# Kernel optimization log

Hardware: AMD Instinct MI355X
Metric: run time of the kernel (lower is better)

The kernel has to match this reference:

```python
import jax, jax.numpy as jnp
import numpy as np

N_MODEL = 1024
N_HEADS = 16
KV_HEADS = 4
HEAD_DIM = N_MODEL // N_HEADS          # 64
KV_MODEL = HEAD_DIM * KV_HEADS         # 256
GROUPS = N_HEADS // KV_HEADS           # 4
B, S = 4, 2048


def _rmsnorm(x):
    return x * jax.lax.rsqrt(jnp.mean(x * x, axis=-1, keepdims=True) + 1e-6)


def _act_quant(x):
    # 8-bit absmax per-token quantization (BitNet b1.58)
    scale = 127.0 / jnp.clip(jnp.max(jnp.abs(x), axis=-1, keepdims=True), 1e-5)
    return jnp.clip(jnp.round(x * scale), -128.0, 127.0) / scale


def _weight_quant(w):
    # ternary absmean quantization
    scale = 1.0 / jnp.clip(jnp.mean(jnp.abs(w)), 1e-5)
    return jnp.clip(jnp.round(w * scale), -1.0, 1.0) / scale


def bitlinear(x, w, b):
    xn = _rmsnorm(x)
    xq = xn + jax.lax.stop_gradient(_act_quant(xn) - xn)   # STE
    wq = w + jax.lax.stop_gradient(_weight_quant(w) - w)   # STE
    return jnp.einsum('...i,oi->...o', xq, wq) + b


def setup_inputs() -> dict:
    key = jax.random.key(0)
    ks = jax.random.split(key, 11)
    sq = 1.0 / np.sqrt(N_MODEL)
    sk = 1.0 / np.sqrt(KV_MODEL)
    return {
        'query': jax.random.normal(ks[0], (B, S, N_MODEL), jnp.float32),
        'key':   jax.random.normal(ks[1], (B, S, N_MODEL), jnp.float32),
        'value': jax.random.normal(ks[2], (B, S, N_MODEL), jnp.float32),
        'Wq': jax.random.normal(ks[3], (N_MODEL, N_MODEL), jnp.float32) * sq,
        'bq': jnp.zeros((N_MODEL,), jnp.float32),
        'Wk': jax.random.normal(ks[4], (KV_MODEL, N_MODEL), jnp.float32) * sq,
        'bk': jnp.zeros((KV_MODEL,), jnp.float32),
        'Wv': jax.random.normal(ks[5], (KV_MODEL, N_MODEL), jnp.float32) * sq,
        'bv': jnp.zeros((KV_MODEL,), jnp.float32),
        'Wo': jax.random.normal(ks[6], (N_MODEL, KV_MODEL), jnp.float32) * sk,
        'bo': jnp.zeros((N_MODEL,), jnp.float32),
    }


def reference(query, key, value, Wq, bq, Wk, bk, Wv, bv, Wo, bo):
    b = query.shape[0]
    Q = bitlinear(query, Wq, bq)   # [b, n, n_model]
    K = bitlinear(key,   Wk, bk)   # [b, s, kv_model]
    V = bitlinear(value, Wv, bv)   # [b, s, kv_model]

    # [b, h, n, d] layouts
    Q = Q.reshape(b, -1, N_HEADS, HEAD_DIM).transpose(0, 2, 1, 3)
    K = K.reshape(b, -1, KV_HEADS, HEAD_DIM).transpose(0, 2, 1, 3)
    V = V.reshape(b, -1, KV_HEADS, HEAD_DIM).transpose(0, 2, 1, 3)

    # group query heads: [b, g, kv_h, n, d]
    Qg = Q.reshape(b, KV_HEADS, GROUPS, -1, HEAD_DIM).transpose(0, 2, 1, 3, 4)
    # NOTE: faithful to the module, the einsum output has no 'g' axis,
    # so the grouped query heads are SUMMED over g.
    energy = jnp.einsum('bghnd,bhsd->bhns', Qg, K)  # [b, kv_h, n, s]

    scale = jnp.sqrt(jnp.float32(HEAD_DIM))
    attention = jax.nn.softmax(energy / scale, axis=-1)
    x = jnp.einsum('bhns,bhsd->bhnd', attention, V)  # [b, kv_h, n, d]
    x = x.transpose(0, 2, 1, 3).reshape(b, -1, KV_MODEL)
    x = bitlinear(x, Wo, bo)       # [b, n, n_model]
    return (x, attention)
```

## Files before the change

### kernel.cpp

```cpp
#include <hip/hip_runtime.h>
#include <stdint.h>

#define N_MODELC 1024
#define KV_MODELC 256
#define BATCH 4
#define SEQ 2048
#define NTOK (BATCH*SEQ)
#define NCHUNK 4
#define CHUNK (SEQ/NCHUNK)

typedef __attribute__((ext_vector_type(4))) float f32x4;
typedef __attribute__((ext_vector_type(4))) int   i32x4;
typedef __attribute__((ext_vector_type(8))) short s16x8;
typedef __attribute__((ext_vector_type(4))) short s16x4;

__device__ __forceinline__ unsigned short f2bf(float f){
  unsigned u = __builtin_bit_cast(unsigned, f);
  u = (u + 0x7FFFu + ((u>>16)&1u)) >> 16;
  return (unsigned short)u;
}
__device__ __forceinline__ float bf2f(unsigned short b){
  return __builtin_bit_cast(float, ((unsigned)b)<<16);
}

__global__ __launch_bounds__(256) void k_actquant1024(
    const float* __restrict__ xq_in, const float* __restrict__ xk_in, const float* __restrict__ xv_in,
    int8_t* __restrict__ q8q, int8_t* __restrict__ q8k, int8_t* __restrict__ q8v,
    float* __restrict__ scq, float* __restrict__ sck, float* __restrict__ scv)
{
  int row = blockIdx.x, which = blockIdx.y, t = threadIdx.x;
  const float* x = (which==0)?xq_in:(which==1)?xk_in:xv_in;
  int8_t* q8 = (which==0)?q8q:(which==1)?q8k:q8v;
  float* sc = (which==0)?scq:(which==1)?sck:scv;
  const float* xr = x + (size_t)row*N_MODELC;
  float4 v = reinterpret_cast<const float4*>(xr)[t];
  float ss = v.x*v.x + v.y*v.y + v.z*v.z + v.w*v.w;
  float am = fmaxf(fmaxf(fabsf(v.x),fabsf(v.y)), fmaxf(fabsf(v.z),fabsf(v.w)));
  #pragma unroll
  for (int m=32;m;m>>=1){ ss += __shfl_xor(ss,m,64); am = fmaxf(am, __shfl_xor(am,m,64)); }
  __shared__ float red[8];
  int wid = t>>6;
  if ((t&63)==0){ red[wid]=ss; red[4+wid]=am; }
  __syncthreads();
  ss = red[0]+red[1]+red[2]+red[3];
  am = fmaxf(fmaxf(red[4],red[5]), fmaxf(red[6],red[7]));
  float rinv = rsqrtf(ss*(1.0f/N_MODELC) + 1e-6f);
  float clipv = fmaxf(am*rinv, 1e-5f);
  float qs = 127.0f/clipv;
  float fsc = rinv*qs;
  char4 o;
  o.x = (signed char)(int)fminf(127.f, fmaxf(-128.f, rintf(v.x*fsc)));
  o.y = (signed char)(int)fminf(127.f, fmaxf(-128.f, rintf(v.y*fsc)));
  o.z = (signed char)(int)fminf(127.f, fmaxf(-128.f, rintf(v.z*fsc)));
  o.w = (signed char)(int)fminf(127.f, fmaxf(-128.f, rintf(v.w*fsc)));
  reinterpret_cast<char4*>(q8 + (size_t)row*N_MODELC)[t] = o;
  if (t==0) sc[row] = clipv*(1.0f/127.0f);
}

__global__ __launch_bounds__(64) void k_actquant256(
    const float* __restrict__ X, int8_t* __restrict__ q8, float* __restrict__ sc)
{
  int row = blockIdx.x, l = threadIdx.x;
  float4 v = reinterpret_cast<const float4*>(X + (size_t)row*KV_MODELC)[l];
  float ss = v.x*v.x + v.y*v.y + v.z*v.z + v.w*v.w;
  float am = fmaxf(fmaxf(fabsf(v.x),fabsf(v.y)), fmaxf(fabsf(v.z),fabsf(v.w)));
  #pragma unroll
  for (int m=32;m;m>>=1){ ss += __shfl_xor(ss,m,64); am = fmaxf(am, __shfl_xor(am,m,64)); }
  float rinv = rsqrtf(ss*(1.0f/KV_MODELC) + 1e-6f);
  float clipv = fmaxf(am*rinv, 1e-5f);
  float qs = 127.0f/clipv;
  float fsc = rinv*qs;
  char4 o;
  o.x = (signed char)(int)fminf(127.f, fmaxf(-128.f, rintf(v.x*fsc)));
  o.y = (signed char)(int)fminf(127.f, fmaxf(-128.f, rintf(v.y*fsc)));
  o.z = (signed char)(int)fminf(127.f, fmaxf(-128.f, rintf(v.z*fsc)));
  o.w = (signed char)(int)fminf(127.f, fmaxf(-128.f, rintf(v.w*fsc)));
  reinterpret_cast<char4*>(q8 + (size_t)row*KV_MODELC)[l] = o;
  if (l==0) sc[row] = clipv*(1.0f/127.0f);
}

__global__ __launch_bounds__(256) void k_wabs_partial(
    const float* __restrict__ Wq, const float* __restrict__ Wk,
    const float* __restrict__ Wv, const float* __restrict__ Wo, float* __restrict__ partial)
{
  int mat = blockIdx.y;
  const float* w = (mat==0)?Wq:(mat==1)?Wk:(mat==2)?Wv:Wo;
  int n = (mat==0)?(N_MODELC*N_MODELC):(KV_MODELC*N_MODELC);
  float s = 0.f;
  for (int i = blockIdx.x*256 + threadIdx.x; i < n; i += 256*256) s += fabsf(w[i]);
  #pragma unroll
  for (int m=32;m;m>>=1) s += __shfl_xor(s,m,64);
  __shared__ float red[4];
  int wid = threadIdx.x>>6;
  if ((threadIdx.x&63)==0) red[wid]=s;
  __syncthreads();
  if (threadIdx.x==0) partial[mat*256 + blockIdx.x] = red[0]+red[1]+red[2]+red[3];
}

__global__ __launch_bounds__(256) void k_wfinal(const float* __restrict__ partial, float* __restrict__ wfac)
{
  int mat = blockIdx.x, t = threadIdx.x;
  float s = partial[mat*256 + t];
  #pragma unroll
  for (int m=32;m;m>>=1) s += __shfl_xor(s,m,64);
  __shared__ float red[4];
  int wid = t>>6;
  if ((t&63)==0) red[wid]=s;
  __syncthreads();
  if (t==0){
    float tot = red[0]+red[1]+red[2]+red[3];
    float n = (mat==0)?(float)(N_MODELC*N_MODELC):(float)(KV_MODELC*N_MODELC);
    wfac[mat] = fmaxf(tot/n, 1e-5f);
  }
}

__global__ __launch_bounds__(256) void k_tern(
    const float* __restrict__ Wq, const float* __restrict__ Wk,
    const float* __restrict__ Wv, const float* __restrict__ Wo,
    const float* __restrict__ wfac,
    int8_t* __restrict__ Wqs, int8_t* __restrict__ Wkt,
    int8_t* __restrict__ Wvt, int8_t* __restrict__ Wot)
{
  int mat = blockIdx.y;
  int idx = blockIdx.x*256 + threadIdx.x;
  if (mat==0){
    float s = 1.0f/wfac[0];
    int op = idx>>10, i = idx&1023;
    int kv = op>>6, d = op&63;
    int acc = 0;
    #pragma unroll
    for (int g=0; g<4; g++){
      float w = Wq[(size_t)(kv*256 + g*64 + d)*N_MODELC + i];
      float r = fminf(1.f, fmaxf(-1.f, rintf(w*s)));
      acc += (int)r;
    }
    Wqs[idx] = (int8_t)acc;
  } else {
    const float* w = (mat==1)?Wk:(mat==2)?Wv:Wo;
    int8_t* o = (mat==1)?Wkt:(mat==2)?Wvt:Wot;
    float s = 1.0f/wfac[mat];
    float r = fminf(1.f, fmaxf(-1.f, rintf(w[idx]*s)));
    o[idx] = (int8_t)r;
  }
}

template<int MODE>
__global__ __launch_bounds__(512) void k_gemm_i8_1024(
    const int8_t* __restrict__ A, const int8_t* __restrict__ B,
    const float* __restrict__ rowscale, const float* __restrict__ wfac, int wfi,
    const float* __restrict__ bias, unsigned short* __restrict__ outp)
{
  __shared__ i32x4 redk[4][4][64];
  __shared__ unsigned short tlds[(MODE==2)?64:1][72];
  const int KDIM = 1024;
  int mb = blockIdx.x*64, nb = blockIdx.y*64;
  int w = threadIdx.x>>6, l = threadIdx.x&63, lr = l&15, lk = l>>4;
  int rw = w&3, kh = w>>2;
  const int8_t* Ap = A + (size_t)(mb + rw*16 + lr)*KDIM + kh*512 + lk*16;
  const int8_t* Bp = B + (size_t)(nb + lr)*KDIM + kh*512 + lk*16;
  i32x4 acc[4];
  #pragma unroll
  for (int f=0; f<4; f++) acc[f] = i32x4{0,0,0,0};
  #pragma unroll 4
  for (int kk=0; kk<512; kk+=64){
    i32x4 a = *reinterpret_cast<const i32x4*>(Ap + kk);
    #pragma unroll
    for (int f=0; f<4; f++){
      i32x4 b = *reinterpret_cast<const i32x4*>(Bp + (size_t)f*16*KDIM + kk);
      acc[f] = __builtin_amdgcn_mfma_i32_16x16x64_i8(a, b, acc[f], 0, 0, 0);
    }
  }
  if (kh==1){
    #pragma unroll
    for (int f=0; f<4; f++) redk[rw][f][l] = acc[f];
  }
  __syncthreads();
  if (kh==0){
    float wf = wfac[wfi];
    #pragma unroll
    for (int f=0; f<4; f++){
      acc[f] += redk[rw][f][l];
      int col = nb + f*16 + lr;
      float bval;
      if constexpr (MODE==0){
        int kv = col>>6, d = col&63;
        const float* bb = bias + kv*256 + d;
        bval = bb[0]+bb[64]+bb[128]+bb[192];
      } else {
        bval = bias[col];
      }
      #pragma unroll
      for (int r=0; r<4; r++){
        int row = mb + rw*16 + lk*4 + r;
        float val = (float)acc[f][r] * (rowscale[row]*wf) + bval;
        if constexpr (MODE==0){
          outp[(size_t)row*KV_MODELC + col] = f2bf(0.125f*val);
        } else if constexpr (MODE==1){
          outp[(size_t)row*KV_MODELC + col] = f2bf(val);
        } else {
          tlds[f*16+lr][rw*16 + lk*4 + r] = f2bf(val);
        }
      }
    }
  }
  if constexpr (MODE==2){
    __syncthreads();
    int u = threadIdx.x;
    int col = u>>3, part = u&7;
    int b = mb>>11, s0 = mb&2047;
    s16x8 vv = *reinterpret_cast<const s16x8*>(&tlds[col][part*8]);
    *reinterpret_cast<s16x8*>(&outp[((size_t)(b*256 + nb + col))*SEQ + s0 + part*8]) = vv;
  }
}

__global__ __launch_bounds__(256) void k_gemm_o(
    const int8_t* __restrict__ A, const int8_t* __restrict__ B,
    const float* __restrict__ rowscale, const float* __restrict__ wfac,
    const float* __restrict__ bias, float* __restrict__ outp)
{
  const int KDIM = 256;
  int mb = blockIdx.x*64, nb = blockIdx.y*64;
  int w = threadIdx.x>>6, l = threadIdx.x&63, lr = l&15, lk = l>>4;
  const int8_t* Ap = A + (size_t)(mb + w*16 + lr)*KDIM + lk*16;
  const int8_t* Bp = B + (size_t)(nb + lr)*KDIM + lk*16;
  i32x4 acc[4];
  #pragma unroll
  for (int f=0; f<4; f++) acc[f] = i32x4{0,0,0,0};
  #pragma unroll
  for (int kk=0; kk<KDIM; kk+=64){
    i32x4 a = *reinterpret_cast<const i32x4*>(Ap + kk);
    #pragma unroll
    for (int f=0; f<4; f++){
      i32x4 b = *reinterpret_cast<const i32x4*>(Bp + (size_t)f*16*KDIM + kk);
      acc[f] = __builtin_amdgcn_mfma_i32_16x16x64_i8(a, b, acc[f], 0, 0, 0);
    }
  }
  float wf = wfac[3];
  #pragma unroll
  for (int f=0; f<4; f++){
    int col = nb + f*16 + lr;
    float bval = bias[col];
    #pragma unroll
    for (int r=0; r<4; r++){
      int row = mb + w*16 + lk*4 + r;
      outp[(size_t)row*N_MODELC + col] = (float)acc[f][r]*(rowscale[row]*wf) + bval;
    }
  }
}

__global__ __launch_bounds__(256) void k_attn1(
    const unsigned short* __restrict__ Qs, const unsigned short* __restrict__ Kb,
    float* __restrict__ mpart, float* __restrict__ lpart)
{
  int bkv = blockIdx.y, b = bkv>>2, kv = bkv&3;
  int c = blockIdx.z;
  int w = threadIdx.x>>6, l = threadIdx.x&63, lr = l&15, lk = l>>4;
  int rowt = blockIdx.x*64 + w*16;
  size_t tq = (size_t)(b*SEQ + rowt + lr)*KV_MODELC + kv*64 + lk*8;
  s16x8 qa0 = *reinterpret_cast<const s16x8*>(Qs + tq);
  s16x8 qa1 = *reinterpret_cast<const s16x8*>(Qs + tq + 32);
  const unsigned short* kbase = Kb + (size_t)b*SEQ*KV_MODELC + kv*64 + lk*8;
  float m[4], ll[4];
  #pragma unroll
  for (int r=0;r<4;r++){ m[r] = -INFINITY; ll[r] = 0.f; }
  for (int st=c*CHUNK; st<(c+1)*CHUNK; st+=16){
    const unsigned short* kp = kbase + (size_t)(st+lr)*KV_MODELC;
    s16x8 k0 = *reinterpret_cast<const s16x8*>(kp);
    s16x8 k1 = *reinterpret_cast<const s16x8*>(kp + 32);
    f32x4 acc = {0.f,0.f,0.f,0.f};
    acc = __builtin_amdgcn_mfma_f32_16x16x32_bf16(qa0, k0, acc, 0,0,0);
    acc = __builtin_amdgcn_mfma_f32_16x16x32_bf16(qa1, k1, acc, 0,0,0);
    #pragma unroll
    for (int r=0;r<4;r++){
      float e = acc[r];
      float mn = fmaxf(m[r], e);
      ll[r] = ll[r]*__expf(m[r]-mn) + __expf(e-mn);
      m[r] = mn;
    }
  }
  #pragma unroll
  for (int r=0;r<4;r++){
    #pragma unroll
    for (int mask=1; mask<16; mask<<=1){
      float om = __shfl_xor(m[r], mask, 64);
      float ol = __shfl_xor(ll[r], mask, 64);
      float mn = fmaxf(m[r], om);
      ll[r] = ll[r]*__expf(m[r]-mn) + ol*__expf(om-mn);
      m[r] = mn;
    }
  }
  if (lr==0){
    #pragma unroll
    for (int r=0;r<4;r++){
      size_t idx = ((size_t)(c*16 + bkv))*SEQ + rowt + lk*4 + r;
      mpart[idx] = m[r];
      lpart[idx] = ll[r];
    }
  }
}

__global__ __launch_bounds__(256) void k_attn2(
    const unsigned short* __restrict__ Qs, const unsigned short* __restrict__ Kb,
    const unsigned short* __restrict__ VT,
    const float* __restrict__ mpart, const float* __restrict__ lpart,
    float* __restrict__ attn, float* __restrict__ pvpart)
{
  __shared__ unsigned short plds[64][64];
  int bkv = blockIdx.y, b = bkv>>2, kv = bkv&3;
  int c = blockIdx.z;
  int w = threadIdx.x>>6, l = threadIdx.x&63, lr = l&15, lk = l>>4;
  int brow = blockIdx.x*64;
  int rowt = brow + w*16;
  size_t tq = (size_t)(b*SEQ + rowt + lr)*KV_MODELC + kv*64 + lk*8;
  s16x8 qa0 = *reinterpret_cast<const s16x8*>(Qs + tq);
  s16x8 qa1 = *reinterpret_cast<const s16x8*>(Qs + tq + 32);
  const unsigned short* kbase = Kb + (size_t)b*SEQ*KV_MODELC + kv*64 + lk*8;
  const unsigned short* vbase = VT + ((size_t)(b*256 + kv*64))*SEQ;

  float m[4], invl[4];
  #pragma unroll
  for (int r=0;r<4;r++){
    int row = rowt + lk*4 + r;
    float M = -INFINITY, L = 0.f;
    #pragma unroll
    for (int cc=0; cc<NCHUNK; cc++){
      size_t idx = ((size_t)(cc*16 + bkv))*SEQ + row;
      float mm = mpart[idx], lw = lpart[idx];
      float mn = fmaxf(M, mm);
      L = L*__expf(M-mn) + lw*__expf(mm-mn);
      M = mn;
    }
    m[r] = M; invl[r] = 1.0f/L;
  }

  float* arow = attn + (size_t)bkv*SEQ*SEQ + (size_t)brow*SEQ;
  f32x4 acco[4];
  #pragma unroll
  for (int dt=0; dt<4; dt++) acco[dt] = f32x4{0.f,0.f,0.f,0.f};
  int qw = w*16 + lk*4;
  int qr = w*16 + lr;
  int rsw = (qr&7)<<3;

  for (int st=c*CHUNK; st<(c+1)*CHUNK; st+=64){
    #pragma unroll
    for (int sub=0; sub<4; sub++){
      int s0 = st + sub*16;
      const unsigned short* kp = kbase + (size_t)(s0+lr)*KV_MODELC;
      s16x8 k0 = *reinterpret_cast<const s16x8*>(kp);
      s16x8 k1 = *reinterpret_cast<const s16x8*>(kp + 32);
      f32x4 acc = {0.f,0.f,0.f,0.f};
      acc = __builtin_amdgcn_mfma_f32_16x16x32_bf16(qa0, k0, acc, 0,0,0);
      acc = __builtin_amdgcn_mfma_f32_16x16x32_bf16(qa1, k1, acc, 0,0,0);
      int slocal = sub*16 + lr;
      #pragma unroll
      for (int r=0;r<4;r++){
        float p = __expf(acc[r]-m[r])*invl[r];
        int sw = (slocal & 7) | ((((slocal>>3) ^ ((qw+r)&7)))<<3);
        plds[qw + r][sw] = f2bf(p);
      }
    }
    s16x8 a0 = *reinterpret_cast<const s16x8*>(&plds[qr][(lk<<3) ^ rsw]);
    s16x8 a1 = *reinterpret_cast<const s16x8*>(&plds[qr][((4+lk)<<3) ^ rsw]);
    #pragma unroll
    for (int dt=0; dt<4; dt++){
      const unsigned short* vp = vbase + (size_t)(dt*16+lr)*SEQ + st + lk*8;
      s16x8 b0 = *reinterpret_cast<const s16x8*>(vp);
      s16x8 b1 = *reinterpret_cast<const s16x8*>(vp + 32);
      acco[dt] = __builtin_amdgcn_mfma_f32_16x16x32_bf16(a0, b0, acco[dt], 0,0,0);
      acco[dt] = __builtin_amdgcn_mfma_f32_16x16x32_bf16(a1, b1, acco[dt], 0,0,0);
    }
    #pragma unroll
    for (int j=0; j<4; j++){
      int row = w*16 + j*4 + (l>>4);
      int sseg = l & 15;
      int chunk = sseg >> 1, half = sseg & 1;
      int off = ((chunk ^ (row&7)) << 3) + (half<<2);
      s16x4 pb = *reinterpret_cast<const s16x4*>(&plds[row][off]);
      float4 pv4;
      pv4.x = bf2f((unsigned short)pb[0]);
      pv4.y = bf2f((unsigned short)pb[1]);
      pv4.z = bf2f((unsigned short)pb[2]);
      pv4.w = bf2f((unsigned short)pb[3]);
      *reinterpret_cast<float4*>(&arow[(size_t)row*SEQ + st + sseg*4]) = pv4;
    }
  }
  {
    int T = (bkv*32 + blockIdx.x)*4 + w;
    float* base = pvpart + ((size_t)c*2048 + T)*1024;
    #pragma unroll
    for (int dt=0; dt<4; dt++){
      *reinterpret_cast<f32x4*>(base + (dt*64 + l)*4) = acco[dt];
    }
  }
}

__global__ __launch_bounds__(256) void k_pvsum(
    const float* __restrict__ pvpart, float* __restrict__ X)
{
  __shared__ float xls[16][65];
  int T = blockIdx.x;
  int w = T&3, qblk = (T>>2)&31, bkv = T>>7;
  int b = bkv>>2, kv = bkv&3;
  int t = threadIdx.x;
  int dt = t>>6, l = t&63;
  f32x4 s = {0.f,0.f,0.f,0.f};
  #pragma unroll
  for (int c=0; c<NCHUNK; c++){
    f32x4 v = *reinterpret_cast<const f32x4*>(pvpart + ((size_t)c*2048 + T)*1024 + t*4);
    s += v;
  }
  int lk = l>>4, lr = l&15;
  #pragma unroll
  for (int r=0; r<4; r++) xls[lk*4+r][dt*16+lr] = s[r];
  __syncthreads();
  int row = t>>4, col4 = (t&15)*4;
  float4 o;
  o.x = xls[row][col4]; o.y = xls[row][col4+1];
  o.z = xls[row][col4+2]; o.w = xls[row][col4+3];
  *reinterpret_cast<float4*>(&X[((size_t)(b*SEQ + qblk*64 + w*16 + row))*KV_MODELC + kv*64 + col4]) = o;
}

extern "C" void kernel_launch(void* const* d_in, const int* in_sizes, int n_in,
                              void* d_out, int out_size, void* d_ws, size_t ws_size,
                              hipStream_t stream)
{
  (void)in_sizes; (void)n_in; (void)out_size; (void)ws_size;
  const float* q  = (const float*)d_in[0];
  const float* k  = (const float*)d_in[1];
  const float* v  = (const float*)d_in[2];
  const float* Wq = (const float*)d_in[3];
  const float* bq = (const float*)d_in[4];
  const float* Wk = (const float*)d_in[5];
  const float* bk = (const float*)d_in[6];
  const float* Wv = (const float*)d_in[7];
  const float* bv = (const float*)d_in[8];
  const float* Wo = (const float*)d_in[9];
  const float* bo = (const float*)d_in[10];

  float* out_x = (float*)d_out;
  float* out_attn = out_x + (size_t)NTOK*N_MODELC;

  char* ws = (char*)d_ws;
  size_t off = 0;
  auto alloc = [&](size_t bytes)->void*{
    void* p = ws + off; off += (bytes + 255) & ~(size_t)255; return p;
  };
  int8_t* q8q = (int8_t*)alloc((size_t)NTOK*N_MODELC);
  int8_t* q8k = (int8_t*)alloc((size_t)NTOK*N_MODELC);
  int8_t* q8v = (int8_t*)alloc((size_t)NTOK*N_MODELC);
  int8_t* q8x = (int8_t*)alloc((size_t)NTOK*KV_MODELC);
  float* scq = (float*)alloc(NTOK*4);
  float* sck = (float*)alloc(NTOK*4);
  float* scv = (float*)alloc(NTOK*4);
  float* scx = (float*)alloc(NTOK*4);
  float* partial = (float*)alloc(4*256*4);
  float* wfac = (float*)alloc(256);
  int8_t* Wqs = (int8_t*)alloc(256*1024);
  int8_t* Wkt = (int8_t*)alloc(256*1024);
  int8_t* Wvt = (int8_t*)alloc(256*1024);
  int8_t* Wot = (int8_t*)alloc(1024*256);
  unsigned short* Qs = (unsigned short*)alloc((size_t)NTOK*KV_MODELC*2);
  unsigned short* Kb = (unsigned short*)alloc((size_t)NTOK*KV_MODELC*2);
  unsigned short* VT = (unsigned short*)alloc((size_t)NTOK*KV_MODELC*2);
  float* X = (float*)alloc((size_t)NTOK*KV_MODELC*4);
  float* mpart = (float*)alloc((size_t)NCHUNK*16*SEQ*4);
  float* lpart = (float*)alloc((size_t)NCHUNK*16*SEQ*4);
  float* pvpart = (float*)alloc((size_t)NCHUNK*2048*1024*4);

  hipLaunchKernelGGL(k_actquant1024, dim3(NTOK,3), dim3(256), 0, stream,
                     q,k,v, q8q,q8k,q8v, scq,sck,scv);
  hipLaunchKernelGGL(k_wabs_partial, dim3(256,4), dim3(256), 0, stream, Wq,Wk,Wv,Wo, partial);
  hipLaunchKernelGGL(k_wfinal, dim3(4), dim3(256), 0, stream, partial, wfac);
  hipLaunchKernelGGL(k_tern, dim3(1024,4), dim3(256), 0, stream,
                     Wq,Wk,Wv,Wo, wfac, Wqs,Wkt,Wvt,Wot);
  hipLaunchKernelGGL((k_gemm_i8_1024<0>), dim3(128,4), dim3(512), 0, stream,
                     q8q, Wqs, scq, wfac, 0, bq, Qs);
  hipLaunchKernelGGL((k_gemm_i8_1024<1>), dim3(128,4), dim3(512), 0, stream,
                     q8k, Wkt, sck, wfac, 1, bk, Kb);
  hipLaunchKernelGGL((k_gemm_i8_1024<2>), dim3(128,4), dim3(512), 0, stream,
                     q8v, Wvt, scv, wfac, 2, bv, VT);
  hipLaunchKernelGGL(k_attn1, dim3(32,16,NCHUNK), dim3(256), 0, stream,
                     Qs, Kb, mpart, lpart);
  hipLaunchKernelGGL(k_attn2, dim3(32,16,NCHUNK), dim3(256), 0, stream,
                     Qs, Kb, VT, mpart, lpart, out_attn, pvpart);
  hipLaunchKernelGGL(k_pvsum, dim3(2048), dim3(256), 0, stream, pvpart, X);
  hipLaunchKernelGGL(k_actquant256, dim3(NTOK), dim3(64), 0, stream, X, q8x, scx);
  hipLaunchKernelGGL(k_gemm_o, dim3(128,16), dim3(256), 0, stream,
                     q8x, Wot, scx, wfac, bo, out_x);
}
```

Baseline: 336.3 us.

## Fuse two-pass attention into single pass with fixed softmax shift

```diff
diff --git a/kernel.cpp b/kernel.cpp
--- a/kernel.cpp
+++ b/kernel.cpp
@@ -6,13 +6,13 @@
 #define BATCH 4
 #define SEQ 2048
 #define NTOK (BATCH*SEQ)
-#define NCHUNK 4
-#define CHUNK (SEQ/NCHUNK)
 
 typedef __attribute__((ext_vector_type(4))) float f32x4;
 typedef __attribute__((ext_vector_type(4))) int   i32x4;
 typedef __attribute__((ext_vector_type(8))) short s16x8;
-typedef __attribute__((ext_vector_type(4))) short s16x4;
+
+#define LOG2E 1.4426950408889634f
+#define PSHIFT 32.0f
 
 __device__ __forceinline__ unsigned short f2bf(float f){
   unsigned u = __builtin_bit_cast(unsigned, f);
@@ -248,66 +248,14 @@
   }
 }
 
-__global__ __launch_bounds__(256) void k_attn1(
+__global__ __launch_bounds__(256) void k_attn_fused(
     const unsigned short* __restrict__ Qs, const unsigned short* __restrict__ Kb,
-    float* __restrict__ mpart, float* __restrict__ lpart)
-{
+    const unsigned short* __restrict__ VT, unsigned short* __restrict__ Pws,
+    float* __restrict__ attn, float* __restrict__ X)
+{
+  __shared__ unsigned short plds[64][64];
+  __shared__ float linvl[64];
   int bkv = blockIdx.y, b = bkv>>2, kv = bkv&3;
-  int c = blockIdx.z;
-  int w = threadIdx.x>>6, l = threadIdx.x&63, lr = l&15, lk = l>>4;
-  int rowt = blockIdx.x*64 + w*16;
-  size_t tq = (size_t)(b*SEQ + rowt + lr)*KV_MODELC + kv*64 + lk*8;
-  s16x8 qa0 = *reinterpret_cast<const s16x8*>(Qs + tq);
-  s16x8 qa1 = *reinterpret_cast<const s16x8*>(Qs + tq + 32);
-  const unsigned short* kbase = Kb + (size_t)b*SEQ*KV_MODELC + kv*64 + lk*8;
-  float m[4], ll[4];
-  #pragma unroll
-  for (int r=0;r<4;r++){ m[r] = -INFINITY; ll[r] = 0.f; }
-  for (int st=c*CHUNK; st<(c+1)*CHUNK; st+=16){
-    const unsigned short* kp = kbase + (size_t)(st+lr)*KV_MODELC;
-    s16x8 k0 = *reinterpret_cast<const s16x8*>(kp);
-    s16x8 k1 = *reinterpret_cast<const s16x8*>(kp + 32);
-    f32x4 acc = {0.f,0.f,0.f,0.f};
-    acc = __builtin_amdgcn_mfma_f32_16x16x32_bf16(qa0, k0, acc, 0,0,0);
-    acc = __builtin_amdgcn_mfma_f32_16x16x32_bf16(qa1, k1, acc, 0,0,0);
-    #pragma unroll
-    for (int r=0;r<4;r++){
-      float e = acc[r];
-      float mn = fmaxf(m[r], e);
-      ll[r] = ll[r]*__expf(m[r]-mn) + __expf(e-mn);
-      m[r] = mn;
-    }
-  }
-  #pragma unroll
-  for (int r=0;r<4;r++){
-    #pragma unroll
-    for (int mask=1; mask<16; mask<<=1){
-      float om = __shfl_xor(m[r], mask, 64);
-      float ol = __shfl_xor(ll[r], mask, 64);
-      float mn = fmaxf(m[r], om);
-      ll[r] = ll[r]*__expf(m[r]-mn) + ol*__expf(om-mn);
-      m[r] = mn;
-    }
-  }
-  if (lr==0){
-    #pragma unroll
-    for (int r=0;r<4;r++){
-      size_t idx = ((size_t)(c*16 + bkv))*SEQ + rowt + lk*4 + r;
-      mpart[idx] = m[r];
-      lpart[idx] = ll[r];
-    }
-  }
-}
-
-__global__ __launch_bounds__(256) void k_attn2(
-    const unsigned short* __restrict__ Qs, const unsigned short* __restrict__ Kb,
-    const unsigned short* __restrict__ VT,
-    const float* __restrict__ mpart, const float* __restrict__ lpart,
-    float* __restrict__ attn, float* __restrict__ pvpart)
-{
-  __shared__ unsigned short plds[64][64];
-  int bkv = blockIdx.y, b = bkv>>2, kv = bkv&3;
-  int c = blockIdx.z;
   int w = threadIdx.x>>6, l = threadIdx.x&63, lr = l&15, lk = l>>4;
   int brow = blockIdx.x*64;
   int rowt = brow + w*16;
@@ -316,32 +264,24 @@
   s16x8 qa1 = *reinterpret_cast<const s16x8*>(Qs + tq + 32);
   const unsigned short* kbase = Kb + (size_t)b*SEQ*KV_MODELC + kv*64 + lk*8;
   const unsigned short* vbase = VT + ((size_t)(b*256 + kv*64))*SEQ;
-
-  float m[4], invl[4];
-  #pragma unroll
-  for (int r=0;r<4;r++){
-    int row = rowt + lk*4 + r;
-    float M = -INFINITY, L = 0.f;
-    #pragma unroll
-    for (int cc=0; cc<NCHUNK; cc++){
-      size_t idx = ((size_t)(cc*16 + bkv))*SEQ + row;
-      float mm = mpart[idx], lw = lpart[idx];
-      float mn = fmaxf(M, mm);
-      L = L*__expf(M-mn) + lw*__expf(mm-mn);
-      M = mn;
-    }
-    m[r] = M; invl[r] = 1.0f/L;
-  }
-
-  float* arow = attn + (size_t)bkv*SEQ*SEQ + (size_t)brow*SEQ;
+  unsigned short* pblk = Pws + ((size_t)(bkv*32 + blockIdx.x))*64*SEQ;
+
+  s16x8 ones;
+  #pragma unroll
+  for (int i=0;i<8;i++) ones[i] = (short)0x3F80;
+
   f32x4 acco[4];
   #pragma unroll
   for (int dt=0; dt<4; dt++) acco[dt] = f32x4{0.f,0.f,0.f,0.f};
+  f32x4 accl = {0.f,0.f,0.f,0.f};
+
   int qw = w*16 + lk*4;
   int qr = w*16 + lr;
-  int rsw = (qr&7)<<3;
-
-  for (int st=c*CHUNK; st<(c+1)*CHUNK; st+=64){
+  int rsw = (lr&7)<<3;
+  int rbrow = w*16 + (l>>2);
+  int rbb = l&3;
+
+  for (int st=0; st<SEQ; st+=64){
     #pragma unroll
     for (int sub=0; sub<4; sub++){
       int s0 = st + sub*16;
@@ -354,13 +294,15 @@
       int slocal = sub*16 + lr;
       #pragma unroll
       for (int r=0;r<4;r++){
-        float p = __expf(acc[r]-m[r])*invl[r];
+        float p = exp2f(fmaf(acc[r], LOG2E, -PSHIFT));
         int sw = (slocal & 7) | ((((slocal>>3) ^ ((qw+r)&7)))<<3);
         plds[qw + r][sw] = f2bf(p);
       }
     }
     s16x8 a0 = *reinterpret_cast<const s16x8*>(&plds[qr][(lk<<3) ^ rsw]);
     s16x8 a1 = *reinterpret_cast<const s16x8*>(&plds[qr][((4+lk)<<3) ^ rsw]);
+    accl = __builtin_amdgcn_mfma_f32_16x16x32_bf16(a0, ones, accl, 0,0,0);
+    accl = __builtin_amdgcn_mfma_f32_16x16x32_bf16(a1, ones, accl, 0,0,0);
     #pragma unroll
     for (int dt=0; dt<4; dt++){
       const unsigned short* vp = vbase + (size_t)(dt*16+lr)*SEQ + st + lk*8;
@@ -369,55 +311,52 @@
       acco[dt] = __builtin_amdgcn_mfma_f32_16x16x32_bf16(a0, b0, acco[dt], 0,0,0);
       acco[dt] = __builtin_amdgcn_mfma_f32_16x16x32_bf16(a1, b1, acco[dt], 0,0,0);
     }
-    #pragma unroll
-    for (int j=0; j<4; j++){
-      int row = w*16 + j*4 + (l>>4);
-      int sseg = l & 15;
-      int chunk = sseg >> 1, half = sseg & 1;
-      int off = ((chunk ^ (row&7)) << 3) + (half<<2);
-      s16x4 pb = *reinterpret_cast<const s16x4*>(&plds[row][off]);
-      float4 pv4;
-      pv4.x = bf2f((unsigned short)pb[0]);
-      pv4.y = bf2f((unsigned short)pb[1]);
-      pv4.z = bf2f((unsigned short)pb[2]);
-      pv4.w = bf2f((unsigned short)pb[3]);
-      *reinterpret_cast<float4*>(&arow[(size_t)row*SEQ + st + sseg*4]) = pv4;
-    }
-  }
-  {
-    int T = (bkv*32 + blockIdx.x)*4 + w;
-    float* base = pvpart + ((size_t)c*2048 + T)*1024;
-    #pragma unroll
-    for (int dt=0; dt<4; dt++){
-      *reinterpret_cast<f32x4*>(base + (dt*64 + l)*4) = acco[dt];
-    }
-  }
-}
-
-__global__ __launch_bounds__(256) void k_pvsum(
-    const float* __restrict__ pvpart, float* __restrict__ X)
-{
-  __shared__ float xls[16][65];
-  int T = blockIdx.x;
-  int w = T&3, qblk = (T>>2)&31, bkv = T>>7;
-  int b = bkv>>2, kv = bkv&3;
+    unsigned short* ptile = pblk + (size_t)(st>>6)*4096;
+    #pragma unroll
+    for (int j8=0; j8<2; j8++){
+      int chunk = rbb*2 + j8;
+      s16x8 v = *reinterpret_cast<const s16x8*>(&plds[rbrow][(chunk ^ (rbrow&7))<<3]);
+      *reinterpret_cast<s16x8*>(&ptile[rbrow*64 + chunk*8]) = v;
+    }
+  }
+
+  float invr[4];
+  #pragma unroll
+  for (int r=0;r<4;r++) invr[r] = 1.0f/accl[r];
+  if (lr==0){
+    #pragma unroll
+    for (int r=0;r<4;r++) linvl[w*16 + lk*4 + r] = invr[r];
+  }
+  int token = b*SEQ + rowt + lk*4;
+  #pragma unroll
+  for (int dt=0; dt<4; dt++){
+    #pragma unroll
+    for (int r=0; r<4; r++){
+      X[(size_t)(token + r)*KV_MODELC + kv*64 + dt*16 + lr] = acco[dt][r]*invr[r];
+    }
+  }
+  __syncthreads();
+
+  float* arow = attn + (size_t)bkv*SEQ*SEQ + (size_t)brow*SEQ;
   int t = threadIdx.x;
-  int dt = t>>6, l = t&63;
-  f32x4 s = {0.f,0.f,0.f,0.f};
-  #pragma unroll
-  for (int c=0; c<NCHUNK; c++){
-    f32x4 v = *reinterpret_cast<const f32x4*>(pvpart + ((size_t)c*2048 + T)*1024 + t*4);
-    s += v;
-  }
-  int lk = l>>4, lr = l&15;
-  #pragma unroll
-  for (int r=0; r<4; r++) xls[lk*4+r][dt*16+lr] = s[r];
-  __syncthreads();
-  int row = t>>4, col4 = (t&15)*4;
-  float4 o;
-  o.x = xls[row][col4]; o.y = xls[row][col4+1];
-  o.z = xls[row][col4+2]; o.w = xls[row][col4+3];
-  *reinterpret_cast<float4*>(&X[((size_t)(b*SEQ + qblk*64 + w*16 + row))*KV_MODELC + kv*64 + col4]) = o;
+  const unsigned short* prd = pblk + (size_t)(t>>3)*4096 + (t&7)*8;
+  #pragma unroll 4
+  for (int it=0; it<64; it++){
+    float inv = linvl[it];
+    s16x8 pv = *reinterpret_cast<const s16x8*>(prd + it*64);
+    float4 o0, o1;
+    o0.x = bf2f((unsigned short)pv[0])*inv;
+    o0.y = bf2f((unsigned short)pv[1])*inv;
+    o0.z = bf2f((unsigned short)pv[2])*inv;
+    o0.w = bf2f((unsigned short)pv[3])*inv;
+    o1.x = bf2f((unsigned short)pv[4])*inv;
+    o1.y = bf2f((unsigned short)pv[5])*inv;
+    o1.z = bf2f((unsigned short)pv[6])*inv;
+    o1.w = bf2f((unsigned short)pv[7])*inv;
+    float* dst = &arow[(size_t)it*SEQ + t*8];
+    *reinterpret_cast<float4*>(dst) = o0;
+    *reinterpret_cast<float4*>(dst+4) = o1;
+  }
 }
 
 extern "C" void kernel_launch(void* const* d_in, const int* in_sizes, int n_in,
@@ -463,9 +402,7 @@
   unsigned short* Kb = (unsigned short*)alloc((size_t)NTOK*KV_MODELC*2);
   unsigned short* VT = (unsigned short*)alloc((size_t)NTOK*KV_MODELC*2);
   float* X = (float*)alloc((size_t)NTOK*KV_MODELC*4);
-  float* mpart = (float*)alloc((size_t)NCHUNK*16*SEQ*4);
-  float* lpart = (float*)alloc((size_t)NCHUNK*16*SEQ*4);
-  float* pvpart = (float*)alloc((size_t)NCHUNK*2048*1024*4);
+  unsigned short* Pws = (unsigned short*)alloc((size_t)16*SEQ*SEQ*2);
 
   hipLaunchKernelGGL(k_actquant1024, dim3(NTOK,3), dim3(256), 0, stream,
                      q,k,v, q8q,q8k,q8v, scq,sck,scv);
@@ -479,11 +416,8 @@
                      q8k, Wkt, sck, wfac, 1, bk, Kb);
   hipLaunchKernelGGL((k_gemm_i8_1024<2>), dim3(128,4), dim3(512), 0, stream,
                      q8v, Wvt, scv, wfac, 2, bv, VT);
-  hipLaunchKernelGGL(k_attn1, dim3(32,16,NCHUNK), dim3(256), 0, stream,
-                     Qs, Kb, mpart, lpart);
-  hipLaunchKernelGGL(k_attn2, dim3(32,16,NCHUNK), dim3(256), 0, stream,
-                     Qs, Kb, VT, mpart, lpart, out_attn, pvpart);
-  hipLaunchKernelGGL(k_pvsum, dim3(2048), dim3(256), 0, stream, pvpart, X);
+  hipLaunchKernelGGL(k_attn_fused, dim3(32,16), dim3(256), 0, stream,
+                     Qs, Kb, VT, Pws, out_attn, X);
   hipLaunchKernelGGL(k_actquant256, dim3(NTOK), dim3(64), 0, stream, X, q8x, scx);
   hipLaunchKernelGGL(k_gemm_o, dim3(128,16), dim3(256), 0, stream,
                      q8x, Wot, scx, wfac, bo, out_x);
```

Measured after the change: 351.4 us. +4.5%, slower.
